# Kernel optimization log

Hardware: AMD Instinct MI355X
Metric: run time of the kernel (lower is better)

## Reference

```python
import jax, jax.numpy as jnp
import numpy as np

ZDIM, NF, H, S, B = 64, 32, 256, 256, 1024


def setup_inputs() -> dict:
    key = jax.random.key(0)
    ks = jax.random.split(key, 8)
    def w(k, shape, fan):
        return (jax.random.normal(k, shape, jnp.float32) / np.sqrt(fan)).astype(jnp.float32)
    return {
        "z": jax.random.normal(ks[0], (B, ZDIM), jnp.float32),
        "W_lat": w(ks[1], (2 * H, ZDIM), ZDIM),
        "b_lat": jnp.zeros((2 * H,), jnp.float32),
        "W_ih": w(ks[2], (4 * H, NF), NF),
        "b_ih": jnp.zeros((4 * H,), jnp.float32),
        "W_hh": w(ks[3], (4 * H, H), H),
        "b_hh": jnp.zeros((4 * H,), jnp.float32),
        "W_out": w(ks[4], (NF, H), H),
        "b_out": jnp.zeros((NF,), jnp.float32),
        "W_sig": w(ks[5], (NF, H * S), H * S),
        "b_sig": jnp.zeros((NF,), jnp.float32),
    }


def reference(z, W_lat, b_lat, W_ih, b_ih, W_hh, b_hh, W_out, b_out, W_sig, b_sig):
    # from_latent: split into initial hidden / cell state
    hc = z @ W_lat.T + b_lat                      # [B, 2H]
    h, c = hc[:, :H], hc[:, H:]
    x = jnp.zeros((z.shape[0], NF), z.dtype)      # initial LSTM input
    bias = b_ih + b_hh                            # fold both LSTM biases

    def step(carry, _):
        h, c, x = carry
        g = x @ W_ih.T + h @ W_hh.T + bias        # [B, 4H]; torch gate order i,f,g,o
        i, f, gg, o = jnp.split(g, 4, axis=-1)
        c = jax.nn.sigmoid(f) * c + jax.nn.sigmoid(i) * jnp.tanh(gg)
        h = jax.nn.sigmoid(o) * jnp.tanh(c)
        x_next = jnp.tanh(h) @ W_out.T + b_out    # activation(Tanh) then from_lstm
        return (h, c, x_next), (h, x_next)

    _, (hs, mus) = jax.lax.scan(step, (h, c, x), None, length=S)
    # mus: [S, B, NF] -> mu: [B, NF, S]
    mu = jnp.transpose(mus, (1, 2, 0))
    # hs: [S, B, H] -> [B, H, S] -> flatten hidden-major, matching torch permute+reshape
    xs = jnp.transpose(hs, (1, 2, 0)).reshape(-1, H * S)
    sigma = jax.nn.softplus(xs @ W_sig.T + b_sig)[:, :, None]   # [B, NF, 1]
    return (mu, sigma)
```

## Files before the change

### kernel.cpp

```cpp
#include <hip/hip_runtime.h>

#define NF 32
#define HDIM 256
#define SLEN 256
#define BATCH 1024

typedef float f32x4 __attribute__((ext_vector_type(4)));
typedef __bf16 bf16x8 __attribute__((ext_vector_type(8)));
typedef unsigned int u32x4 __attribute__((ext_vector_type(4)));
typedef unsigned short u16;

#define MFMA __builtin_amdgcn_mfma_f32_16x16x32_bf16

#define WHH_O 0
#define WIH_O 32768
#define WOUT_O 36864
#define WLAT_O 37888
#define PREP1_N 41984
#define WT_BYTE (1u << 20)
#define HST_BYTE (8u << 20)

__device__ __forceinline__ u16 f2bf(float x) {
  __bf16 b = (__bf16)x;
  return __builtin_bit_cast(u16, b);
}
__device__ __forceinline__ unsigned int pk2(float a, float b) {
  return (unsigned int)f2bf(a) | ((unsigned int)f2bf(b) << 16);
}
__device__ __forceinline__ float sigf(float x) {
  return __fdividef(1.0f, 1.0f + __expf(-x));
}
__device__ __forceinline__ float tanhf_(float x) {
  return 1.0f - __fdividef(2.0f, __expf(2.0f * x) + 1.0f);
}

__global__ void prep_weights(const float* __restrict__ Whh, const float* __restrict__ Wih,
                             const float* __restrict__ Wout, const float* __restrict__ Wlat,
                             uint4* __restrict__ ws) {
  int i = blockIdx.x * 256 + threadIdx.x;
  if (i >= PREP1_N) return;
  int l = i & 63;
  int c16 = l & 15, g4 = l >> 4;
  const float* src;
  if (i < WIH_O) {
    int t = (i >> 6) & 7, j = i >> 9;
    src = Whh + (j * 16 + c16) * 256 + t * 32 + 8 * g4;
  } else if (i < WOUT_O) {
    int ii = i - WIH_O;
    int j = ii >> 6;
    src = Wih + (j * 16 + c16) * 32 + 8 * g4;
  } else if (i < WLAT_O) {
    int ii = i - WOUT_O;
    int t = (ii >> 6) & 7, j = ii >> 9;
    src = Wout + (j * 16 + c16) * 256 + t * 32 + 8 * g4;
  } else {
    int ii = i - WLAT_O;
    int t = (ii >> 6) & 1, j = ii >> 7;
    src = Wlat + (j * 16 + c16) * 64 + t * 32 + 8 * g4;
  }
  uint4 P;
  P.x = pk2(src[0], src[1]);
  P.y = pk2(src[2], src[3]);
  P.z = pk2(src[4], src[5]);
  P.w = pk2(src[6], src[7]);
  ws[i] = P;
}

__global__ void prep_wt(const float* __restrict__ Wsig, unsigned short* __restrict__ Wt) {
  __shared__ float tile[32][257];
  int f = blockIdx.x >> 3, hb = blockIdx.x & 7;
  int tid = threadIdx.x;
  const float* src = Wsig + f * (HDIM * SLEN) + hb * 32 * 256;
#pragma unroll
  for (int i = 0; i < 32; ++i) tile[i][tid] = src[i * 256 + tid];
  __syncthreads();
  int s = tid;
  unsigned short tmp[32];
#pragma unroll
  for (int h = 0; h < 32; ++h) tmp[h] = f2bf(tile[h][s]);
  uint4* dst = (uint4*)(Wt + f * 65536 + s * 256 + hb * 32);
  const uint4* tsrc = (const uint4*)tmp;
#pragma unroll
  for (int j = 0; j < 4; ++j) dst[j] = tsrc[j];
}

__global__ __launch_bounds__(1024, 4) void lstm_scan(
    const float* __restrict__ z, const float* __restrict__ b_lat,
    const float* __restrict__ b_ih, const float* __restrict__ b_hh,
    const float* __restrict__ b_out,
    const uint4* __restrict__ ws, unsigned short* __restrict__ hst,
    float* __restrict__ out) {
  __shared__ __align__(16) uint4 wihl[4096];
  __shared__ __align__(16) uint4 woutb[1024];
  __shared__ __align__(16) u16 hbuf[2][16][256];
  __shared__ __align__(16) u16 thbuf[16][256];
  __shared__ __align__(16) u16 xbuf[2][16][32];
  __shared__ __align__(16) float mubuf[16][16][32];

  const int tid = threadIdx.x, w = tid >> 6, l = tid & 63;
  const int c16 = l & 15, g4 = l >> 4, r0 = g4 * 4;
  const int wg = blockIdx.x;
  const int swz = (c16 & 7) << 3;

  for (int i = tid; i < 4096; i += 1024) wihl[i] = ws[WIH_O + i];
  for (int i = tid; i < 1024; i += 1024) woutb[i] = ws[WOUT_O + i];

  u32x4 wp[4][3];
#pragma unroll
  for (int gi = 0; gi < 4; ++gi)
#pragma unroll
    for (int kk = 0; kk < 3; ++kk)
      wp[gi][kk] = __builtin_bit_cast(u32x4, ws[WHH_O + ((gi * 16 + w) * 8 + kk) * 64 + l]);

  const uint4* bs[4];
#pragma unroll
  for (int gi = 0; gi < 4; ++gi) bs[gi] = ws + WHH_O + ((gi * 16 + w) * 8 + 4) * 64 + l;

  float biasv[4];
#pragma unroll
  for (int gi = 0; gi < 4; ++gi) {
    int n = (gi * 16 + w) * 16 + c16;
    biasv[gi] = b_ih[n] + b_hh[n];
  }
  const int jn = w - 14;
  float bo = (w >= 14) ? b_out[jn * 16 + c16] : 0.f;

  thbuf[tid >> 6][tid & 63] = f2bf(z[(wg * 16 + (tid >> 6)) * 64 + (tid & 63)]);
  if (tid < 512) xbuf[0][tid >> 5][tid & 31] = 0;
  __syncthreads();

  float cst[4];
  {
    bf16x8 za0 = *reinterpret_cast<const bf16x8*>(&thbuf[c16][8 * g4]);
    bf16x8 za1 = *reinterpret_cast<const bf16x8*>(&thbuf[c16][32 + 8 * g4]);
    float blh = b_lat[w * 16 + c16];
    float blc = b_lat[256 + w * 16 + c16];
    f32x4 ah = {blh, blh, blh, blh}, ac = {blc, blc, blc, blc};
    ah = MFMA(za0, *reinterpret_cast<const bf16x8*>(ws + WLAT_O + (w * 2 + 0) * 64 + l), ah, 0, 0, 0);
    ah = MFMA(za1, *reinterpret_cast<const bf16x8*>(ws + WLAT_O + (w * 2 + 1) * 64 + l), ah, 0, 0, 0);
    ac = MFMA(za0, *reinterpret_cast<const bf16x8*>(ws + WLAT_O + ((16 + w) * 2 + 0) * 64 + l), ac, 0, 0, 0);
    ac = MFMA(za1, *reinterpret_cast<const bf16x8*>(ws + WLAT_O + ((16 + w) * 2 + 1) * 64 + l), ac, 0, 0, 0);
    const int hc = w * 16 + c16;
#pragma unroll
    for (int v = 0; v < 4; ++v) {
      cst[v] = ac[v];
      int rr = r0 + v;
      hbuf[0][rr][hc ^ ((rr & 7) << 3)] = f2bf(ah[v]);
    }
  }
  __syncthreads();

  for (int s = 0; s < SLEN; ++s) {
    const int pb = s & 1;
    f32x4 acc[4];
#pragma unroll
    for (int gi = 0; gi < 4; ++gi)
      acc[gi] = (f32x4){biasv[gi], biasv[gi], biasv[gi], biasv[gi]};
#pragma unroll
    for (int kt = 0; kt < 8; ++kt) {
      bf16x8 afr = *reinterpret_cast<const bf16x8*>(&hbuf[pb][c16][(kt * 32 + 8 * g4) ^ swz]);
      if (kt < 3) {
#pragma unroll
        for (int gi = 0; gi < 4; ++gi)
          acc[gi] = MFMA(afr, __builtin_bit_cast(bf16x8, wp[gi][kt]), acc[gi], 0, 0, 0);
      } else {
#pragma unroll
        for (int gi = 0; gi < 4; ++gi)
          acc[gi] = MFMA(afr, *reinterpret_cast<const bf16x8*>(bs[gi] + (kt - 4) * 64), acc[gi], 0, 0, 0);
      }
    }
    {
      bf16x8 xfr = *reinterpret_cast<const bf16x8*>(&xbuf[pb][c16][8 * g4]);
#pragma unroll
      for (int gi = 0; gi < 4; ++gi)
        acc[gi] = MFMA(xfr, *reinterpret_cast<const bf16x8*>(&wihl[(gi * 16 + w) * 64 + l]), acc[gi], 0, 0, 0);
    }
    {
      const int hc = w * 16 + c16;
#pragma unroll
      for (int v = 0; v < 4; ++v) {
        float iv = acc[0][v];
        float fv = acc[1][v];
        float gv = acc[2][v];
        float ov = acc[3][v];
        float cc = sigf(fv) * cst[v] + sigf(iv) * tanhf_(gv);
        cst[v] = cc;
        float hh = sigf(ov) * tanhf_(cc);
        float th = tanhf_(hh);
        int rr = r0 + v;
        int sc = hc ^ ((rr & 7) << 3);
        hbuf[pb ^ 1][rr][sc] = f2bf(hh);
        thbuf[rr][sc] = f2bf(th);
      }
    }
    __syncthreads();
    if (w >= 14) {
      f32x4 xacc = {bo, bo, bo, bo};
#pragma unroll
      for (int t = 0; t < 8; ++t) {
        bf16x8 ta = *reinterpret_cast<const bf16x8*>(&thbuf[c16][(t * 32 + 8 * g4) ^ swz]);
        xacc = MFMA(ta, *reinterpret_cast<const bf16x8*>(&woutb[(jn * 8 + t) * 64 + l]), xacc, 0, 0, 0);
      }
      const int f = jn * 16 + c16;
      const int sw = s & 15;
#pragma unroll
      for (int v = 0; v < 4; ++v) {
        int rr = r0 + v;
        xbuf[pb ^ 1][rr][f] = f2bf(xacc[v]);
        mubuf[sw][rr][f] = xacc[v];
      }
    } else if (w < 8) {
      int r = tid >> 5;
      int h0 = (tid & 31) * 8;
      uint4 d = *reinterpret_cast<const uint4*>(&hbuf[pb ^ 1][r][h0 ^ ((r & 7) << 3)]);
      *reinterpret_cast<uint4*>(hst + ((wg * 16 + r) << 16) + (s << 8) + h0) = d;
    }
    __syncthreads();
    if ((s & 15) == 15 && tid < 512) {
      int b = tid >> 5, f = tid & 31;
      float* dst = out + ((wg * 16 + b) << 13) + (f << 8) + (s - 15);
#pragma unroll
      for (int j4 = 0; j4 < 4; ++j4) {
        f32x4 vv;
#pragma unroll
        for (int jj = 0; jj < 4; ++jj) vv[jj] = mubuf[j4 * 4 + jj][b][f];
        *reinterpret_cast<f32x4*>(dst + j4 * 4) = vv;
      }
    }
#pragma unroll
    for (int gi = 0; gi < 4; ++gi)
#pragma unroll
      for (int kk = 0; kk < 3; ++kk)
        asm volatile("" : "+v"(wp[gi][kk]));
  }
}

__global__ __launch_bounds__(512) void sigma_gemm(
    const unsigned short* __restrict__ hst, const unsigned short* __restrict__ Wt,
    const float* __restrict__ b_sig, float* __restrict__ out) {
  __shared__ float sred[8][16][32];
  const int tid = threadIdx.x;
  const int w = tid >> 6;
  const int l = tid & 63;
  const int c16 = l & 15;
  const int g4 = l >> 4;
  const int wg = blockIdx.x;

  const unsigned short* ap =
      hst + (((wg << 2) + (c16 & 3)) << 16) + ((w * 32) << 8) + (g4 << 3);
  const unsigned short* bp0 = Wt + (c16 << 16) + ((w * 32) << 8) + (g4 << 3);
  const unsigned short* bp1 = Wt + ((16 + c16) << 16) + ((w * 32) << 8) + (g4 << 3);

  f32x4 a0 = {0.f, 0.f, 0.f, 0.f}, a1 = {0.f, 0.f, 0.f, 0.f};
#pragma unroll 8
  for (int kk = 0; kk < 256; ++kk) {
    int off = ((kk >> 3) << 8) + ((kk & 7) << 5);
    bf16x8 av = *reinterpret_cast<const bf16x8*>(ap + off);
    a0 = MFMA(av, *reinterpret_cast<const bf16x8*>(bp0 + off), a0, 0, 0, 0);
    a1 = MFMA(av, *reinterpret_cast<const bf16x8*>(bp1 + off), a1, 0, 0, 0);
  }
#pragma unroll
  for (int v = 0; v < 4; ++v) {
    sred[w][g4 * 4 + v][c16] = a0[v];
    sred[w][g4 * 4 + v][16 + c16] = a1[v];
  }
  __syncthreads();
  int b = tid >> 5, f = tid & 31;
  if (b < 4) {
    float acc = b_sig[f];
#pragma unroll
    for (int ww = 0; ww < 8; ++ww) acc += sred[ww][b][f];
    float sp = fmaxf(acc, 0.0f) + log1pf(__expf(-fabsf(acc)));
    out[BATCH * NF * SLEN + ((wg << 2) + b) * NF + f] = sp;
  }
}

extern "C" void kernel_launch(void* const* d_in, const int* in_sizes, int n_in,
                              void* d_out, int out_size, void* d_ws, size_t ws_size,
                              hipStream_t stream) {
  (void)in_sizes; (void)n_in; (void)out_size; (void)ws_size;
  const float* z     = (const float*)d_in[0];
  const float* W_lat = (const float*)d_in[1];
  const float* b_lat = (const float*)d_in[2];
  const float* W_ih  = (const float*)d_in[3];
  const float* b_ih  = (const float*)d_in[4];
  const float* W_hh  = (const float*)d_in[5];
  const float* b_hh  = (const float*)d_in[6];
  const float* W_out = (const float*)d_in[7];
  const float* b_out = (const float*)d_in[8];
  const float* W_sig = (const float*)d_in[9];
  const float* b_sig = (const float*)d_in[10];
  char* wsb = (char*)d_ws;
  uint4* ws = (uint4*)wsb;
  unsigned short* Wt  = (unsigned short*)(wsb + WT_BYTE);
  unsigned short* hst = (unsigned short*)(wsb + HST_BYTE);
  float* out = (float*)d_out;

  prep_weights<<<(PREP1_N + 255) / 256, 256, 0, stream>>>(W_hh, W_ih, W_out, W_lat, ws);
  prep_wt<<<256, 256, 0, stream>>>(W_sig, Wt);
  lstm_scan<<<64, 1024, 0, stream>>>(z, b_lat, b_ih, b_hh, b_out, ws, hst, out);
  sigma_gemm<<<256, 512, 0, stream>>>(hst, Wt, b_sig, out);
}
```

Measured before the change: 3.102 ms.

## Overlap output projection and h-state stores with recurrent gate MFMAs

Restructures the LSTM step loop so the output projection (x_next / mu) from the previous step runs on waves 14-15 at the start of the next step, overlapping the W_hh MFMAs of the other waves. The hst store of the previous step's h is moved the same way. The x buffer becomes single-buffered, and an epilogue after the loop handles the final step. It also pins the cached W_hh fragments to AGPRs via asm constraints and sets explicit waves-per-eu attributes. The aim is to take the serial x-projection phase off the critical path between barriers. The cost is an extra barrier per step and more complex indexing at the loop boundaries.

Result: slower. 3.675 ms (+18.4%).

```diff
diff --git a/kernel.cpp b/kernel.cpp
--- a/kernel.cpp
+++ b/kernel.cpp
@@ -84,7 +84,8 @@
   for (int j = 0; j < 4; ++j) dst[j] = tsrc[j];
 }
 
-__global__ __launch_bounds__(1024, 4) void lstm_scan(
+__global__ __attribute__((amdgpu_flat_work_group_size(1024, 1024)))
+__attribute__((amdgpu_waves_per_eu(4, 4))) void lstm_scan(
     const float* __restrict__ z, const float* __restrict__ b_lat,
     const float* __restrict__ b_ih, const float* __restrict__ b_hh,
     const float* __restrict__ b_out,
@@ -94,7 +95,7 @@
   __shared__ __align__(16) uint4 woutb[1024];
   __shared__ __align__(16) u16 hbuf[2][16][256];
   __shared__ __align__(16) u16 thbuf[16][256];
-  __shared__ __align__(16) u16 xbuf[2][16][32];
+  __shared__ __align__(16) u16 xbuf[16][32];
   __shared__ __align__(16) float mubuf[16][16][32];
 
   const int tid = threadIdx.x, w = tid >> 6, l = tid & 63;
@@ -103,18 +104,14 @@
   const int swz = (c16 & 7) << 3;
 
   for (int i = tid; i < 4096; i += 1024) wihl[i] = ws[WIH_O + i];
-  for (int i = tid; i < 1024; i += 1024) woutb[i] = ws[WOUT_O + i];
-
-  u32x4 wp[4][3];
+  if (tid < 1024) woutb[tid] = ws[WOUT_O + tid];
+
+  u32x4 wpa[12];
 #pragma unroll
   for (int gi = 0; gi < 4; ++gi)
 #pragma unroll
-    for (int kk = 0; kk < 3; ++kk)
-      wp[gi][kk] = __builtin_bit_cast(u32x4, ws[WHH_O + ((gi * 16 + w) * 8 + kk) * 64 + l]);
-
-  const uint4* bs[4];
-#pragma unroll
-  for (int gi = 0; gi < 4; ++gi) bs[gi] = ws + WHH_O + ((gi * 16 + w) * 8 + 4) * 64 + l;
+    for (int kt = 0; kt < 3; ++kt)
+      wpa[gi * 3 + kt] = __builtin_bit_cast(u32x4, ws[WHH_O + ((gi * 16 + w) * 8 + kt) * 64 + l]);
 
   float biasv[4];
 #pragma unroll
@@ -123,10 +120,10 @@
     biasv[gi] = b_ih[n] + b_hh[n];
   }
   const int jn = w - 14;
-  float bo = (w >= 14) ? b_out[jn * 16 + c16] : 0.f;
+  const float bo = (w >= 14) ? b_out[jn * 16 + c16] : 0.f;
 
   thbuf[tid >> 6][tid & 63] = f2bf(z[(wg * 16 + (tid >> 6)) * 64 + (tid & 63)]);
-  if (tid < 512) xbuf[0][tid >> 5][tid & 31] = 0;
+  if (tid < 512) xbuf[tid >> 5][tid & 31] = 0;
   __syncthreads();
 
   float cst[4];
@@ -151,7 +148,22 @@
   __syncthreads();
 
   for (int s = 0; s < SLEN; ++s) {
+#pragma unroll
+    for (int i = 0; i < 12; ++i) asm volatile("" : "+a"(wpa[i]));
+
     const int pb = s & 1;
+    f32x4 xacc;
+    if (w >= 14 && s > 0) {
+      xacc = (f32x4){bo, bo, bo, bo};
+#pragma unroll
+      for (int t = 0; t < 8; ++t) {
+        bf16x8 ta = *reinterpret_cast<const bf16x8*>(&thbuf[c16][(t * 32 + 8 * g4) ^ swz]);
+        xacc = MFMA(ta, *reinterpret_cast<const bf16x8*>(&woutb[(jn * 8 + t) * 64 + l]), xacc, 0, 0, 0);
+      }
+      const int f = jn * 16 + c16;
+#pragma unroll
+      for (int v = 0; v < 4; ++v) xbuf[r0 + v][f] = f2bf(xacc[v]);
+    }
     f32x4 acc[4];
 #pragma unroll
     for (int gi = 0; gi < 4; ++gi)
@@ -162,15 +174,23 @@
       if (kt < 3) {
 #pragma unroll
         for (int gi = 0; gi < 4; ++gi)
-          acc[gi] = MFMA(afr, __builtin_bit_cast(bf16x8, wp[gi][kt]), acc[gi], 0, 0, 0);
+          acc[gi] = MFMA(afr, __builtin_bit_cast(bf16x8, wpa[gi * 3 + kt]), acc[gi], 0, 0, 0);
       } else {
 #pragma unroll
         for (int gi = 0; gi < 4; ++gi)
-          acc[gi] = MFMA(afr, *reinterpret_cast<const bf16x8*>(bs[gi] + (kt - 4) * 64), acc[gi], 0, 0, 0);
+          acc[gi] = MFMA(afr, *reinterpret_cast<const bf16x8*>(ws + WHH_O + ((gi * 16 + w) * 8 + kt) * 64 + l), acc[gi], 0, 0, 0);
       }
     }
+    if (w < 8 && s > 0) {
+      int r = tid >> 5;
+      int h0 = (tid & 31) * 8;
+      uint4 d = *reinterpret_cast<const uint4*>(&hbuf[pb][r][h0 ^ ((r & 7) << 3)]);
+      *reinterpret_cast<uint4*>(hst + ((wg * 16 + r) << 16) + ((s - 1) << 8) + h0) = d;
+    }
+    __syncthreads();
+
     {
-      bf16x8 xfr = *reinterpret_cast<const bf16x8*>(&xbuf[pb][c16][8 * g4]);
+      bf16x8 xfr = *reinterpret_cast<const bf16x8*>(&xbuf[c16][8 * g4]);
 #pragma unroll
       for (int gi = 0; gi < 4; ++gi)
         acc[gi] = MFMA(xfr, *reinterpret_cast<const bf16x8*>(&wihl[(gi * 16 + w) * 64 + l]), acc[gi], 0, 0, 0);
@@ -193,32 +213,17 @@
         thbuf[rr][sc] = f2bf(th);
       }
     }
+    if (w >= 14 && s > 0) {
+      const int f = jn * 16 + c16;
+      const int mi = (s - 1) & 15;
+#pragma unroll
+      for (int v = 0; v < 4; ++v) mubuf[mi][r0 + v][f] = xacc[v];
+    }
     __syncthreads();
-    if (w >= 14) {
-      f32x4 xacc = {bo, bo, bo, bo};
-#pragma unroll
-      for (int t = 0; t < 8; ++t) {
-        bf16x8 ta = *reinterpret_cast<const bf16x8*>(&thbuf[c16][(t * 32 + 8 * g4) ^ swz]);
-        xacc = MFMA(ta, *reinterpret_cast<const bf16x8*>(&woutb[(jn * 8 + t) * 64 + l]), xacc, 0, 0, 0);
-      }
-      const int f = jn * 16 + c16;
-      const int sw = s & 15;
-#pragma unroll
-      for (int v = 0; v < 4; ++v) {
-        int rr = r0 + v;
-        xbuf[pb ^ 1][rr][f] = f2bf(xacc[v]);
-        mubuf[sw][rr][f] = xacc[v];
-      }
-    } else if (w < 8) {
-      int r = tid >> 5;
-      int h0 = (tid & 31) * 8;
-      uint4 d = *reinterpret_cast<const uint4*>(&hbuf[pb ^ 1][r][h0 ^ ((r & 7) << 3)]);
-      *reinterpret_cast<uint4*>(hst + ((wg * 16 + r) << 16) + (s << 8) + h0) = d;
-    }
-    __syncthreads();
-    if ((s & 15) == 15 && tid < 512) {
+
+    if ((s & 15) == 0 && s > 0 && tid < 512) {
       int b = tid >> 5, f = tid & 31;
-      float* dst = out + ((wg * 16 + b) << 13) + (f << 8) + (s - 15);
+      float* dst = out + ((wg * 16 + b) << 13) + (f << 8) + (s - 16);
 #pragma unroll
       for (int j4 = 0; j4 < 4; ++j4) {
         f32x4 vv;
@@ -227,11 +232,36 @@
         *reinterpret_cast<f32x4*>(dst + j4 * 4) = vv;
       }
     }
-#pragma unroll
-    for (int gi = 0; gi < 4; ++gi)
-#pragma unroll
-      for (int kk = 0; kk < 3; ++kk)
-        asm volatile("" : "+v"(wp[gi][kk]));
+  }
+
+  if (w >= 14) {
+    f32x4 xacc = {bo, bo, bo, bo};
+#pragma unroll
+    for (int t = 0; t < 8; ++t) {
+      bf16x8 ta = *reinterpret_cast<const bf16x8*>(&thbuf[c16][(t * 32 + 8 * g4) ^ swz]);
+      xacc = MFMA(ta, *reinterpret_cast<const bf16x8*>(&woutb[(jn * 8 + t) * 64 + l]), xacc, 0, 0, 0);
+    }
+    const int f = jn * 16 + c16;
+#pragma unroll
+    for (int v = 0; v < 4; ++v) mubuf[15][r0 + v][f] = xacc[v];
+  }
+  __syncthreads();
+  if (tid < 512) {
+    int b = tid >> 5, f = tid & 31;
+    float* dst = out + ((wg * 16 + b) << 13) + (f << 8) + 240;
+#pragma unroll
+    for (int j4 = 0; j4 < 4; ++j4) {
+      f32x4 vv;
+#pragma unroll
+      for (int jj = 0; jj < 4; ++jj) vv[jj] = mubuf[j4 * 4 + jj][b][f];
+      *reinterpret_cast<f32x4*>(dst + j4 * 4) = vv;
+    }
+  }
+  if (w < 8) {
+    int r = tid >> 5;
+    int h0 = (tid & 31) * 8;
+    uint4 d = *reinterpret_cast<const uint4*>(&hbuf[0][r][h0 ^ ((r & 7) << 3)]);
+    *reinterpret_cast<uint4*>(hst + ((wg * 16 + r) << 16) + (255 << 8) + h0) = d;
   }
 }
 
```

## Stream W_hh fragments with two-deep register prefetch and use lightweight barriers

Applied to the files above, without the earlier changes.

Stops pinning three k-tiles of W_hh per gate in registers and instead streams every k-tile from global memory, prefetching two tiles ahead in a rotating register pipeline that wraps across timesteps. Replaces __syncthreads with an explicit lgkmcnt wait plus s_barrier, which no longer waits for outstanding global loads, so prefetches can stay in flight across barriers. The aim is to hide global/L2 latency on the serial recurrence. In exchange all W_hh traffic now goes through cache every step instead of partly coming from registers, and the hst global stores are no longer waited on at the barrier (they are not read within the kernel, so this looks safe).

Result: faster. 2.934 ms (-5.4%).

```diff
diff --git a/kernel.cpp b/kernel.cpp
--- a/kernel.cpp
+++ b/kernel.cpp
@@ -7,7 +7,6 @@
 
 typedef float f32x4 __attribute__((ext_vector_type(4)));
 typedef __bf16 bf16x8 __attribute__((ext_vector_type(8)));
-typedef unsigned int u32x4 __attribute__((ext_vector_type(4)));
 typedef unsigned short u16;
 
 #define MFMA __builtin_amdgcn_mfma_f32_16x16x32_bf16
@@ -32,6 +31,11 @@
 }
 __device__ __forceinline__ float tanhf_(float x) {
   return 1.0f - __fdividef(2.0f, __expf(2.0f * x) + 1.0f);
+}
+
+__device__ __forceinline__ void wg_barrier_lds() {
+  asm volatile("s_waitcnt lgkmcnt(0)" ::: "memory");
+  __builtin_amdgcn_s_barrier();
 }
 
 __global__ void prep_weights(const float* __restrict__ Whh, const float* __restrict__ Wih,
@@ -103,18 +107,12 @@
   const int swz = (c16 & 7) << 3;
 
   for (int i = tid; i < 4096; i += 1024) wihl[i] = ws[WIH_O + i];
-  for (int i = tid; i < 1024; i += 1024) woutb[i] = ws[WOUT_O + i];
-
-  u32x4 wp[4][3];
+  if (tid < 1024) woutb[tid] = ws[WOUT_O + tid];
+
+  const uint4* bs[4];
 #pragma unroll
   for (int gi = 0; gi < 4; ++gi)
-#pragma unroll
-    for (int kk = 0; kk < 3; ++kk)
-      wp[gi][kk] = __builtin_bit_cast(u32x4, ws[WHH_O + ((gi * 16 + w) * 8 + kk) * 64 + l]);
-
-  const uint4* bs[4];
-#pragma unroll
-  for (int gi = 0; gi < 4; ++gi) bs[gi] = ws + WHH_O + ((gi * 16 + w) * 8 + 4) * 64 + l;
+    bs[gi] = ws + WHH_O + ((gi * 16 + w) * 8 + 4) * 64 + l;
 
   float biasv[4];
 #pragma unroll
@@ -123,7 +121,7 @@
     biasv[gi] = b_ih[n] + b_hh[n];
   }
   const int jn = w - 14;
-  float bo = (w >= 14) ? b_out[jn * 16 + c16] : 0.f;
+  const float bo = (w >= 14) ? b_out[jn * 16 + c16] : 0.f;
 
   thbuf[tid >> 6][tid & 63] = f2bf(z[(wg * 16 + (tid >> 6)) * 64 + (tid & 63)]);
   if (tid < 512) xbuf[0][tid >> 5][tid & 31] = 0;
@@ -150,6 +148,12 @@
   }
   __syncthreads();
 
+  uint4 pf0[4], pf1[4];
+#pragma unroll
+  for (int gi = 0; gi < 4; ++gi) pf0[gi] = bs[gi][(0 - 4) * 64];
+#pragma unroll
+  for (int gi = 0; gi < 4; ++gi) pf1[gi] = bs[gi][(1 - 4) * 64];
+
   for (int s = 0; s < SLEN; ++s) {
     const int pb = s & 1;
     f32x4 acc[4];
@@ -158,16 +162,16 @@
       acc[gi] = (f32x4){biasv[gi], biasv[gi], biasv[gi], biasv[gi]};
 #pragma unroll
     for (int kt = 0; kt < 8; ++kt) {
+      uint4 pf2[4];
+      const int ktn = (kt + 2) & 7;
+#pragma unroll
+      for (int gi = 0; gi < 4; ++gi) pf2[gi] = bs[gi][(ktn - 4) * 64];
       bf16x8 afr = *reinterpret_cast<const bf16x8*>(&hbuf[pb][c16][(kt * 32 + 8 * g4) ^ swz]);
-      if (kt < 3) {
-#pragma unroll
-        for (int gi = 0; gi < 4; ++gi)
-          acc[gi] = MFMA(afr, __builtin_bit_cast(bf16x8, wp[gi][kt]), acc[gi], 0, 0, 0);
-      } else {
-#pragma unroll
-        for (int gi = 0; gi < 4; ++gi)
-          acc[gi] = MFMA(afr, *reinterpret_cast<const bf16x8*>(bs[gi] + (kt - 4) * 64), acc[gi], 0, 0, 0);
-      }
+#pragma unroll
+      for (int gi = 0; gi < 4; ++gi)
+        acc[gi] = MFMA(afr, __builtin_bit_cast(bf16x8, pf0[gi]), acc[gi], 0, 0, 0);
+#pragma unroll
+      for (int gi = 0; gi < 4; ++gi) { pf0[gi] = pf1[gi]; pf1[gi] = pf2[gi]; }
     }
     {
       bf16x8 xfr = *reinterpret_cast<const bf16x8*>(&xbuf[pb][c16][8 * g4]);
@@ -193,7 +197,7 @@
         thbuf[rr][sc] = f2bf(th);
       }
     }
-    __syncthreads();
+    wg_barrier_lds();
     if (w >= 14) {
       f32x4 xacc = {bo, bo, bo, bo};
 #pragma unroll
@@ -215,7 +219,7 @@
       uint4 d = *reinterpret_cast<const uint4*>(&hbuf[pb ^ 1][r][h0 ^ ((r & 7) << 3)]);
       *reinterpret_cast<uint4*>(hst + ((wg * 16 + r) << 16) + (s << 8) + h0) = d;
     }
-    __syncthreads();
+    wg_barrier_lds();
     if ((s & 15) == 15 && tid < 512) {
       int b = tid >> 5, f = tid & 31;
       float* dst = out + ((wg * 16 + b) << 13) + (f << 8) + (s - 15);
@@ -227,11 +231,6 @@
         *reinterpret_cast<f32x4*>(dst + j4 * 4) = vv;
       }
     }
-#pragma unroll
-    for (int gi = 0; gi < 4; ++gi)
-#pragma unroll
-      for (int kk = 0; kk < 3; ++kk)
-        asm volatile("" : "+v"(wp[gi][kk]));
   }
 }
 
```
